# Optimization experiments

Hardware: AMD Instinct MI355X
Metric: run time of the kernel (lower is better)

Reference implementation:

```python
import jax, jax.numpy as jnp
import numpy as np

N, E, B, DIN, D = 65536, 1048576, 256, 32, 64
NUM_STEPS_MP = 2   # num_step_message_passing
SET2SET_STEPS = 3  # processing_steps
NUM_CLASSES = 4


def setup_inputs() -> dict:
    key = jax.random.key(0)
    ks = jax.random.split(key, 24)
    def gl(k, shape, fan_in):
        return (jax.random.normal(k, shape, jnp.float32) / np.sqrt(fan_in)).astype(jnp.float32)
    x = jax.random.normal(ks[0], (N, DIN), jnp.float32)
    edge_index = jax.random.randint(ks[1], (2, E), 0, N, dtype=jnp.int32).astype(jnp.int64)
    batch = jnp.sort(jax.random.randint(ks[2], (N,), 0, B, dtype=jnp.int32)).astype(jnp.int64)
    inp = dict(
        x=x, edge_index=edge_index, batch=batch,
        # conv1.mlp: Linear(DIN -> D)
        W_mlp=gl(ks[3], (D, DIN), DIN), b_mlp=jnp.zeros((D,), jnp.float32),
        # HenrionConv linear (D -> D), messages scatter-summed over edges
        W_conv=gl(ks[4], (D, D), D), b_conv=jnp.zeros((D,), jnp.float32),
        # GRU(input = D + DIN, hidden = D); gate order r,z,n (PyTorch)
        gru_W_ih=gl(ks[5], (3 * D, D + DIN), D + DIN),
        gru_W_hh=gl(ks[6], (3 * D, D), D),
        gru_b_ih=jnp.zeros((3 * D,), jnp.float32),
        gru_b_hh=jnp.zeros((3 * D,), jnp.float32),
        # Set2Set LSTM(input = 2D, hidden = D); gate order i,f,g,o (PyTorch)
        lstm_W_ih=gl(ks[7], (4 * D, 2 * D), 2 * D),
        lstm_W_hh=gl(ks[8], (4 * D, D), D),
        lstm_b_ih=jnp.zeros((4 * D,), jnp.float32),
        lstm_b_hh=jnp.zeros((4 * D,), jnp.float32),
        # head MLPs
        W1=gl(ks[9], (D, 2 * D), 2 * D), b1=jnp.zeros((D,), jnp.float32),
        W2=gl(ks[10], (NUM_CLASSES, D), D), b2=jnp.zeros((NUM_CLASSES,), jnp.float32),
        num_graphs=B,
    )
    return inp


def _forward(x, edge_index, batch, W_mlp, b_mlp, W_conv, b_conv,
             gru_W_ih, gru_W_hh, gru_b_ih, gru_b_hh,
             lstm_W_ih, lstm_W_hh, lstm_b_ih, lstm_b_hh,
             W1, b1, W2, b2, num_graphs):
    n = x.shape[0]
    d = W_mlp.shape[0]
    src, dst = edge_index[0], edge_index[1]

    # ---- Henrion_MPNNConv ----
    out = x @ W_mlp.T + b_mlp            # [N, D]
    h = out
    for _ in range(NUM_STEPS_MP):
        # HenrionConv: linear on source node features, scatter-sum to destinations
        msg = (out @ W_conv.T + b_conv)[src]               # [E, D] gather
        m = jax.ops.segment_sum(msg, dst, num_segments=n)  # [N, D] scatter
        inp = jnp.concatenate([m, x], axis=-1)             # [N, D+DIN]
        # GRU cell (seq len 1)
        gi = inp @ gru_W_ih.T + gru_b_ih
        gh = h @ gru_W_hh.T + gru_b_hh
        gi_r, gi_z, gi_n = jnp.split(gi, 3, axis=-1)
        gh_r, gh_z, gh_n = jnp.split(gh, 3, axis=-1)
        r = jax.nn.sigmoid(gi_r + gh_r)
        z = jax.nn.sigmoid(gi_z + gh_z)
        ng = jnp.tanh(gi_n + r * gh_n)
        h = (1.0 - z) * ng + z * h
        out = h

    # ---- Set2Set (processing_steps = 3) ----
    bsz = num_graphs
    q_star = jnp.zeros((bsz, 2 * d), out.dtype)
    hl = jnp.zeros((bsz, d), out.dtype)
    cl = jnp.zeros((bsz, d), out.dtype)
    for _ in range(SET2SET_STEPS):
        gates = q_star @ lstm_W_ih.T + lstm_b_ih + hl @ lstm_W_hh.T + lstm_b_hh
        gi, gf, gg, go = jnp.split(gates, 4, axis=-1)
        cl = jax.nn.sigmoid(gf) * cl + jax.nn.sigmoid(gi) * jnp.tanh(gg)
        hl = jax.nn.sigmoid(go) * jnp.tanh(cl)
        q = hl                                             # [B, D]
        e = jnp.sum(out * q[batch], axis=-1)               # [N]
        e_max = jax.ops.segment_max(e, batch, num_segments=bsz)
        e_max = jnp.where(jnp.isfinite(e_max), e_max, 0.0)
        a = jnp.exp(e - e_max[batch])
        a_sum = jax.ops.segment_sum(a, batch, num_segments=bsz)
        a = a / jnp.maximum(a_sum[batch], 1e-16)           # segment softmax
        r = jax.ops.segment_sum(a[:, None] * out, batch, num_segments=bsz)  # [B, D]
        q_star = jnp.concatenate([q, r], axis=-1)          # [B, 2D]

    # ---- head (eval mode: dropout is identity) ----
    hid = jax.nn.relu(q_star @ W1.T + b1)
    logits = hid @ W2.T + b2
    return jax.nn.log_softmax(logits, axis=-1)             # [B, 4]


def reference(x, edge_index, batch, W_mlp, b_mlp, W_conv, b_conv,
              gru_W_ih, gru_W_hh, gru_b_ih, gru_b_hh,
              lstm_W_ih, lstm_W_hh, lstm_b_ih, lstm_b_hh,
              W1, b1, W2, b2, num_graphs):
    return _forward(x, edge_index, batch, W_mlp, b_mlp, W_conv, b_conv,
                    gru_W_ih, gru_W_hh, gru_b_ih, gru_b_hh,
                    lstm_W_ih, lstm_W_hh, lstm_b_ih, lstm_b_hh,
                    W1, b1, W2, b2, num_graphs)
```

## Files before the change

### kernel.cpp

```cpp
#include <hip/hip_runtime.h>
#include <math.h>

constexpr int Nn  = 65536;
constexpr int Ne  = 1048576;
constexpr int Bg  = 256;
constexpr int DIN = 32;
constexpr int D   = 64;

constexpr int NB   = 256;
constexpr int BCAP = 6144;

typedef __attribute__((ext_vector_type(8))) short bf16x8;
typedef __attribute__((ext_vector_type(8))) unsigned short u16x8;
typedef __attribute__((ext_vector_type(4))) float f32x4;

__device__ __forceinline__ float sigf(float x) { return 1.0f / (1.0f + expf(-x)); }

__device__ __forceinline__ unsigned short bf16_rne(float f) {
  unsigned u = __float_as_uint(f);
  unsigned r = u + 0x7FFFu + ((u >> 16) & 1u);
  return (unsigned short)(r >> 16);
}
__device__ __forceinline__ float bf16_tof(unsigned short h) {
  return __uint_as_float(((unsigned)h) << 16);
}
__device__ __forceinline__ void split2(float f, unsigned short& hi, unsigned short& lo) {
  hi = bf16_rne(f);
  lo = bf16_rne(f - bf16_tof(hi));
}
__device__ __forceinline__ float recon(unsigned short hi, unsigned short lo) {
  return bf16_tof(hi) + bf16_tof(lo);
}

#define MFMA(a, b, c) __builtin_amdgcn_mfma_f32_16x16x32_bf16(a, b, c, 0, 0, 0)

__global__ void k_prepw(const float* __restrict__ W_mlp, const float* __restrict__ W_conv,
                        const float* __restrict__ gWih, const float* __restrict__ gWhh,
                        const float* __restrict__ b_conv,
                        const float* __restrict__ lW_ih, const float* __restrict__ lW_hh,
                        const float* __restrict__ W1,
                        unsigned short* __restrict__ mlp_h, unsigned short* __restrict__ mlp_l,
                        unsigned short* __restrict__ gw_h,  unsigned short* __restrict__ gw_l,
                        float* __restrict__ WihT, float* __restrict__ WhhT,
                        float* __restrict__ W1T, float* __restrict__ vfold,
                        const int* __restrict__ batch, int* __restrict__ gp,
                        int* __restrict__ rp) {
  int idx = blockIdx.x * 256 + threadIdx.x;
  if (idx < 30720) {
    int c = idx / 6144, rem = idx % 6144;
    int nt = rem >> 9, lane = (rem >> 3) & 63, j = rem & 7;
    int n = nt * 16 + (lane & 15);
    int kk = c * 32 + (lane >> 4) * 8 + j;
    float v;
    if (c < 2) {
      float s = 0.f;
      for (int o = 0; o < 64; ++o) s = fmaf(gWih[n * 96 + o], W_conv[o * 64 + kk], s);
      v = s;
    } else if (c == 2) {
      v = gWih[n * 96 + kk];
    } else {
      v = gWhh[n * 64 + (c - 3) * 32 + (lane >> 4) * 8 + j];
    }
    unsigned short hi, lo; split2(v, hi, lo);
    gw_h[idx] = hi; gw_l[idx] = lo;
    return;
  }
  if (idx < 32768) {
    int lp = idx - 30720;
    int nt = lp >> 9, lane = (lp >> 3) & 63, j = lp & 7;
    int n = nt * 16 + (lane & 15);
    unsigned short hi, lo;
    split2(W_mlp[n * 32 + (lane >> 4) * 8 + j], hi, lo);
    mlp_h[lp] = hi; mlp_l[lp] = lo;
    return;
  }
  int t = idx - 32768;
  if (t < 32768) {
    int row = t / 128, k = t % 128;
    WihT[k * 256 + row] = lW_ih[t];
  } else if (t < 49152) {
    int j = t - 32768;
    int row = j / 64, k = j % 64;
    WhhT[k * 256 + row] = lW_hh[j];
  } else if (t < 57344) {
    int j = t - 49152;
    int row = j / 128, k = j % 128;
    W1T[k * 64 + row] = W1[j];
  } else if (t < 57344 + Bg + 1) {
    int g = t - 57344;
    if (g == 0) rp[Nn] = Ne;
    int lo = 0, hi = Nn;
    while (lo < hi) {
      int mid = (lo + hi) >> 1;
      if (batch[mid] < g) lo = mid + 1; else hi = mid;
    }
    gp[g] = lo;
  } else if (t < 57344 + 257 + 192) {
    int g = t - 57344 - 257;
    float s = 0.f;
    for (int o = 0; o < 64; ++o) s = fmaf(gWih[g * 96 + o], b_conv[o], s);
    vfold[g] = s;
  }
}

__global__ __launch_bounds__(256) void k_conv1(const float* __restrict__ x,
                                               const unsigned short* __restrict__ Wh,
                                               const unsigned short* __restrict__ Wl,
                                               const float* __restrict__ bias,
                                               unsigned short* __restrict__ hph,
                                               unsigned short* __restrict__ hpl,
                                               unsigned short* __restrict__ Aih,
                                               unsigned short* __restrict__ Ail) {
  int wave = threadIdx.x >> 6, lane = threadIdx.x & 63;
  int quad = lane >> 4;
  int n0w = blockIdx.x * 64 + wave * 16;
  int rowA = n0w + (lane & 15);
  const float4* xp = (const float4*)&x[(size_t)rowA * 32 + quad * 8];
  float4 xa = xp[0], xb = xp[1];
  float xv[8] = {xa.x, xa.y, xa.z, xa.w, xb.x, xb.y, xb.z, xb.w};
  bf16x8 ah, al;
#pragma unroll
  for (int j = 0; j < 8; ++j) {
    unsigned short hi, lo; split2(xv[j], hi, lo);
    ah[j] = (short)hi; al[j] = (short)lo;
  }
  *(bf16x8*)&Aih[(size_t)rowA * 96 + 64 + quad * 8] = ah;
  *(bf16x8*)&Ail[(size_t)rowA * 96 + 64 + quad * 8] = al;

  f32x4 acc[4] = {};
#pragma unroll
  for (int nt = 0; nt < 4; ++nt) {
    bf16x8 bh = *(const bf16x8*)&Wh[(nt * 64 + lane) * 8];
    bf16x8 bl = *(const bf16x8*)&Wl[(nt * 64 + lane) * 8];
    acc[nt] = MFMA(ah, bh, acc[nt]);
    acc[nt] = MFMA(ah, bl, acc[nt]);
    acc[nt] = MFMA(al, bh, acc[nt]);
  }
  int col0 = lane & 15;
#pragma unroll
  for (int nt = 0; nt < 4; ++nt) {
    float bv = bias[nt * 16 + col0];
#pragma unroll
    for (int r = 0; r < 4; ++r) {
      int node = n0w + quad * 4 + r;
      float v = acc[nt][r] + bv;
      size_t o = (size_t)node * 64 + nt * 16 + col0;
      unsigned short hi, lo; split2(v, hi, lo);
      hph[o] = hi; hpl[o] = lo;
    }
  }
}

__global__ __launch_bounds__(256) void k_aggr(const unsigned short* __restrict__ Hh,
                                              const int* __restrict__ rp,
                                              const int* __restrict__ srcs,
                                              unsigned short* __restrict__ Sh,
                                              unsigned short* __restrict__ Sl) {
  int wave = threadIdx.x >> 6, lane = threadIdx.x & 63;
  int node = blockIdx.x * 4 + wave;
  int s = rp[node], e = rp[node + 1];
  int n = e - s;
  const int* sp = srcs + s;
  int col8 = (lane & 7) * 8;
  int eslot = lane >> 3;
  float acc8[8] = {};
  int k = 0;
  for (; k + 16 <= n; k += 16) {
    int sA = sp[k + eslot];
    int sB = sp[k + 8 + eslot];
    u16x8 a = *(const u16x8*)&Hh[(size_t)sA * 64 + col8];
    u16x8 b = *(const u16x8*)&Hh[(size_t)sB * 64 + col8];
#pragma unroll
    for (int j = 0; j < 8; ++j) acc8[j] += bf16_tof(a[j]);
#pragma unroll
    for (int j = 0; j < 8; ++j) acc8[j] += bf16_tof(b[j]);
  }
  for (; k < n; k += 8) {
    if (k + eslot < n) {
      int sA = sp[k + eslot];
      u16x8 a = *(const u16x8*)&Hh[(size_t)sA * 64 + col8];
#pragma unroll
      for (int j = 0; j < 8; ++j) acc8[j] += bf16_tof(a[j]);
    }
  }
#pragma unroll
  for (int m = 8; m <= 32; m <<= 1) {
#pragma unroll
    for (int j = 0; j < 8; ++j) acc8[j] += __shfl_xor(acc8[j], m);
  }
  if (lane < 8) {
    u16x8 hv, lv;
#pragma unroll
    for (int j = 0; j < 8; ++j) {
      unsigned short hi, lo; split2(acc8[j], hi, lo);
      hv[j] = hi; lv[j] = lo;
    }
    *(u16x8*)&Sh[(size_t)node * 64 + col8] = hv;
    *(u16x8*)&Sl[(size_t)node * 64 + col8] = lv;
  }
}

__global__ __launch_bounds__(256, 2) void k_gru(const unsigned short* __restrict__ Aih,
                                                const unsigned short* __restrict__ Ail,
                                                const unsigned short* __restrict__ Hh,
                                                const unsigned short* __restrict__ Hl,
                                                const unsigned short* __restrict__ Sh,
                                                const unsigned short* __restrict__ Sl,
                                                const unsigned short* __restrict__ gw_h,
                                                const unsigned short* __restrict__ gw_l,
                                                const float* __restrict__ b_ih,
                                                const float* __restrict__ b_hh,
                                                const float* __restrict__ vfold,
                                                const int* __restrict__ rp,
                                                unsigned short* __restrict__ nph,
                                                unsigned short* __restrict__ npl) {
  __shared__ unsigned short sW[2][12288];
  int tid = threadIdx.x;
  int wave = tid >> 6, lane = tid & 63;
  int quad = lane >> 4;
  int n0w = blockIdx.x * 128 + wave * 32;
  int rowA0 = n0w + (lane & 15);

  f32x4 acc0[12] = {}, acc1[12] = {};
  f32x4 aN0[4] = {}, aN1[4] = {};

  bf16x8 gvh[3], gvl[3];
#pragma unroll
  for (int j = 0; j < 3; ++j) {
    gvh[j] = *(const bf16x8*)&gw_h[(tid + j * 256) * 8];
    gvl[j] = *(const bf16x8*)&gw_l[(tid + j * 256) * 8];
  }
#pragma unroll
  for (int j = 0; j < 3; ++j) {
    *(bf16x8*)&sW[0][(tid + j * 256) * 8] = gvh[j];
    *(bf16x8*)&sW[0][6144 + (tid + j * 256) * 8] = gvl[j];
  }
  __syncthreads();

#pragma unroll
  for (int c = 0; c < 5; ++c) {
    const int buf = c & 1;
    if (c < 4) {
#pragma unroll
      for (int j = 0; j < 3; ++j) {
        gvh[j] = *(const bf16x8*)&gw_h[(c + 1) * 6144 + (tid + j * 256) * 8];
        gvl[j] = *(const bf16x8*)&gw_l[(c + 1) * 6144 + (tid + j * 256) * 8];
      }
    }
    bf16x8 a0h, a0l, a1h, a1l;
    if (c < 2) {
      size_t b0 = (size_t)rowA0 * 64 + c * 32 + quad * 8;
      size_t b1 = (size_t)(rowA0 + 16) * 64 + c * 32 + quad * 8;
      a0h = *(const bf16x8*)&Sh[b0]; a0l = *(const bf16x8*)&Sl[b0];
      a1h = *(const bf16x8*)&Sh[b1]; a1l = *(const bf16x8*)&Sl[b1];
    } else if (c == 2) {
      size_t b0 = (size_t)rowA0 * 96 + 64 + quad * 8;
      size_t b1 = (size_t)(rowA0 + 16) * 96 + 64 + quad * 8;
      a0h = *(const bf16x8*)&Aih[b0]; a0l = *(const bf16x8*)&Ail[b0];
      a1h = *(const bf16x8*)&Aih[b1]; a1l = *(const bf16x8*)&Ail[b1];
    } else {
      size_t b0 = (size_t)rowA0 * 64 + (c - 3) * 32 + quad * 8;
      size_t b1 = (size_t)(rowA0 + 16) * 64 + (c - 3) * 32 + quad * 8;
      a0h = *(const bf16x8*)&Hh[b0]; a0l = *(const bf16x8*)&Hl[b0];
      a1h = *(const bf16x8*)&Hh[b1]; a1l = *(const bf16x8*)&Hl[b1];
    }
    const unsigned short* sw = sW[buf];
#pragma unroll
    for (int nt = 0; nt < 12; ++nt) {
      bf16x8 bh = *(const bf16x8*)&sw[(nt * 64 + lane) * 8];
      bf16x8 bl = *(const bf16x8*)&sw[6144 + (nt * 64 + lane) * 8];
      if (c < 3 || nt < 8) {
        acc0[nt] = MFMA(a0h, bh, acc0[nt]);
        acc0[nt] = MFMA(a0h, bl, acc0[nt]);
        acc0[nt] = MFMA(a0l, bh, acc0[nt]);
        acc1[nt] = MFMA(a1h, bh, acc1[nt]);
        acc1[nt] = MFMA(a1h, bl, acc1[nt]);
        acc1[nt] = MFMA(a1l, bh, acc1[nt]);
      } else {
        aN0[nt - 8] = MFMA(a0h, bh, aN0[nt - 8]);
        aN0[nt - 8] = MFMA(a0h, bl, aN0[nt - 8]);
        aN0[nt - 8] = MFMA(a0l, bh, aN0[nt - 8]);
        aN1[nt - 8] = MFMA(a1h, bh, aN1[nt - 8]);
        aN1[nt - 8] = MFMA(a1h, bl, aN1[nt - 8]);
        aN1[nt - 8] = MFMA(a1l, bh, aN1[nt - 8]);
      }
    }
    if (c < 4) {
#pragma unroll
      for (int j = 0; j < 3; ++j) {
        *(bf16x8*)&sW[1 - buf][(tid + j * 256) * 8] = gvh[j];
        *(bf16x8*)&sW[1 - buf][6144 + (tid + j * 256) * 8] = gvl[j];
      }
    }
    __syncthreads();
  }

  int col0 = lane & 15;
#pragma unroll
  for (int tile = 0; tile < 2; ++tile) {
    int nb = n0w + tile * 16;
#pragma unroll
    for (int r = 0; r < 4; ++r) {
      int node = nb + quad * 4 + r;
      float degf = (float)(rp[node + 1] - rp[node]);
#pragma unroll
      for (int nt = 0; nt < 4; ++nt) {
        int g = nt * 16 + col0;
        size_t o = (size_t)node * 64 + g;
        float br  = b_ih[g] + b_hh[g] + degf * vfold[g];
        float bz  = b_ih[64 + g] + b_hh[64 + g] + degf * vfold[64 + g];
        float bin = b_ih[128 + g] + degf * vfold[128 + g];
        float bhn = b_hh[128 + g];
        float gr = tile ? acc1[nt][r]     : acc0[nt][r];
        float gz = tile ? acc1[nt + 4][r] : acc0[nt + 4][r];
        float gn = tile ? acc1[nt + 8][r] : acc0[nt + 8][r];
        float hn = tile ? aN1[nt][r]      : aN0[nt][r];
        float rr = sigf(gr + br);
        float zz = sigf(gz + bz);
        float nn = tanhf(gn + bin + rr * (hn + bhn));
        float h_old = recon(Hh[o], Hl[o]);
        float hv = (1.f - zz) * nn + zz * h_old;
        unsigned short hi, lo; split2(hv, hi, lo);
        nph[o] = hi; npl[o] = lo;
      }
    }
  }
}

__global__ __launch_bounds__(256) void k_bucket(const int* __restrict__ eidx,
                                                int* __restrict__ gcur,
                                                int* __restrict__ payload) {
  __shared__ int lcnt[NB];
  __shared__ int lcur[NB];
  int t = threadIdx.x;
  int e0 = blockIdx.x * 4096;
  lcnt[t] = 0;
  __syncthreads();
  int ds[16], ss[16];
#pragma unroll
  for (int i = 0; i < 16; ++i) {
    int e = e0 + i * 256 + t;
    ds[i] = eidx[Ne + e];
    ss[i] = eidx[e];
    atomicAdd(&lcnt[ds[i] >> 8], 1);
  }
  __syncthreads();
  lcur[t] = atomicAdd(&gcur[t * 16], lcnt[t]);
  __syncthreads();
#pragma unroll
  for (int i = 0; i < 16; ++i) {
    int b = ds[i] >> 8;
    int p = atomicAdd(&lcur[b], 1);
    if (p < BCAP) payload[b * BCAP + p] = (ss[i] << 8) | (ds[i] & 255);
  }
}

__global__ __launch_bounds__(256) void k_placeB(const int* __restrict__ gcur,
                                                const int* __restrict__ payload,
                                                int* __restrict__ rp,
                                                int* __restrict__ srcs) {
  __shared__ int sAll[NB];
  __shared__ int hst[NB];
  __shared__ int cur[NB];
  int b = blockIdx.x, t = threadIdx.x;
  sAll[t] = gcur[t * 16];
  hst[t] = 0;
  __syncthreads();
  int cnt = min(sAll[b], BCAP);
  for (int off = 1; off < NB; off <<= 1) {
    int v = (t >= off) ? sAll[t - off] : 0;
    __syncthreads();
    sAll[t] += v;
    __syncthreads();
  }
  int base = sAll[b] - gcur[b * 16];
  const int* pay = &payload[b * BCAP];
  for (int i = t; i < cnt; i += 256) atomicAdd(&hst[pay[i] & 255], 1);
  __syncthreads();
  int c = hst[t];
  cur[t] = c;
  __syncthreads();
  for (int off = 1; off < NB; off <<= 1) {
    int v = (t >= off) ? cur[t - off] : 0;
    __syncthreads();
    cur[t] += v;
    __syncthreads();
  }
  int excl = cur[t] - c;
  rp[b * 256 + t] = base + excl;
  cur[t] = base + excl;
  __syncthreads();
  for (int i = t; i < cnt; i += 256) {
    int pl = pay[i];
    int p = atomicAdd(&cur[pl & 255], 1);
    srcs[p] = pl >> 8;
  }
}

constexpr int LCAP = 448;
constexpr int LPAD = 68;
constexpr int S2T  = 512;
__global__ __launch_bounds__(S2T) void k_s2s(const unsigned short* __restrict__ hph,
                                             const unsigned short* __restrict__ hpl,
                                             const int* __restrict__ gp,
                                             const float* __restrict__ WihT,
                                             const float* __restrict__ WhhT,
                                             const float* __restrict__ b_ih,
                                             const float* __restrict__ b_hh,
                                             const float* __restrict__ W1T,
                                             const float* __restrict__ b1,
                                             const float* __restrict__ W2,
                                             const float* __restrict__ b2,
                                             float* __restrict__ outp) {
  extern __shared__ float hL[];
  int g = blockIdx.x;
  int t = threadIdx.x;
  int w = t >> 6, lane = t & 63;
  __shared__ float qstar_s[128];
  __shared__ float hs[64], cs[64], gates[256];
  __shared__ float eL[LCAP];
  __shared__ float partial[8][64];
  __shared__ float asum_p[8];
  __shared__ float l4[4];
  __shared__ float hid[64];

  if (t < 128) qstar_s[t] = 0.f;
  if (t < 64) { hs[t] = 0.f; cs[t] = 0.f; }
  int s = gp[g], e = gp[g + 1];
  int cnt = e - s;

  {
    int total = cnt * 64;
    for (int j = t * 4; j < total; j += S2T * 4) {
      int nd = j >> 6, col = j & 63;
      ushort4 hh = *(const ushort4*)&hph[(size_t)s * 64 + j];
      ushort4 ll = *(const ushort4*)&hpl[(size_t)s * 64 + j];
      float4 v;
      v.x = recon(hh.x, ll.x); v.y = recon(hh.y, ll.y);
      v.z = recon(hh.z, ll.z); v.w = recon(hh.w, ll.w);
      *(float4*)&hL[nd * LPAD + col] = v;
    }
  }

  for (int it = 0; it < 3; ++it) {
    __syncthreads();

    if (t < 256) {
      float acc = b_ih[t] + b_hh[t];
      for (int k = 0; k < 128; ++k) acc = fmaf(WihT[k * 256 + t], qstar_s[k], acc);
      for (int k = 0; k < 64; ++k)  acc = fmaf(WhhT[k * 256 + t], hs[k], acc);
      gates[t] = acc;
    }
    __syncthreads();
    if (t < 64) {
      float ig = sigf(gates[t]),        fg = sigf(gates[64 + t]);
      float gg = tanhf(gates[128 + t]), og = sigf(gates[192 + t]);
      float c = fg * cs[t] + ig * gg;
      float q = og * tanhf(c);
      cs[t] = c;
      hs[t] = q;
      qstar_s[t] = q;
    }
    __syncthreads();

    int c4 = (lane & 15) * 4;
    float4 qv = {qstar_s[c4], qstar_s[c4 + 1], qstar_s[c4 + 2], qstar_s[c4 + 3]};
    for (int i0 = s + w * 4; i0 < e; i0 += 32) {
      int node = i0 + (lane >> 4);
      float p = 0.f;
      if (node < e) {
        float4 hv = *(const float4*)&hL[(node - s) * LPAD + c4];
        p = hv.x * qv.x + hv.y * qv.y + hv.z * qv.z + hv.w * qv.w;
      }
      p += __shfl_xor(p, 1); p += __shfl_xor(p, 2);
      p += __shfl_xor(p, 4); p += __shfl_xor(p, 8);
      if (node < e && (lane & 15) == 0) eL[node - s] = p;
    }
    __syncthreads();

    float m = -INFINITY;
    for (int i = lane; i < cnt; i += 64) m = fmaxf(m, eL[i]);
#pragma unroll
    for (int o = 32; o >= 1; o >>= 1) m = fmaxf(m, __shfl_xor(m, o));
    float emax = isfinite(m) ? m : 0.f;

    float acc = 0.f, asum = 0.f;
    for (int i = s + w; i < e; i += 8) {
      float a = expf(eL[i - s] - emax);
      asum += a;
      acc = fmaf(a, hL[(i - s) * LPAD + lane], acc);
    }
    partial[w][lane] = acc;
    if (lane == 0) asum_p[w] = asum;
    __syncthreads();
    if (t < 64) {
      float r = 0.f, as = 0.f;
      for (int q = 0; q < 8; ++q) { r += partial[q][t]; as += asum_p[q]; }
      float rv = (cnt > 0) ? r / fmaxf(as, 1e-16f) : 0.f;
      qstar_s[64 + t] = rv;
    }
  }
  __syncthreads();

  if (t < 64) {
    float a1 = b1[t];
    for (int k = 0; k < 64; ++k)   a1 = fmaf(W1T[k * 64 + t], qstar_s[k], a1);
    for (int k = 64; k < 128; ++k) a1 = fmaf(W1T[k * 64 + t], qstar_s[k], a1);
    hid[t] = fmaxf(a1, 0.f);
  }
  __syncthreads();
  if (t < 4) {
    float lg = b2[t];
    for (int d = 0; d < 64; ++d) lg = fmaf(W2[t * 64 + d], hid[d], lg);
    l4[t] = lg;
  }
  __syncthreads();
  if (t < 4) {
    float mx = fmaxf(fmaxf(l4[0], l4[1]), fmaxf(l4[2], l4[3]));
    float ssum = expf(l4[0] - mx) + expf(l4[1] - mx) + expf(l4[2] - mx) + expf(l4[3] - mx);
    outp[g * 4 + t] = l4[t] - mx - logf(ssum);
  }
}

extern "C" void kernel_launch(void* const* d_in, const int* in_sizes, int n_in,
                              void* d_out, int out_size, void* d_ws, size_t ws_size,
                              hipStream_t stream) {
  const float* x        = (const float*)d_in[0];
  const int*   eidx     = (const int*)d_in[1];
  const int*   batch    = (const int*)d_in[2];
  const float* W_mlp    = (const float*)d_in[3];
  const float* b_mlp    = (const float*)d_in[4];
  const float* W_conv   = (const float*)d_in[5];
  const float* b_conv   = (const float*)d_in[6];
  const float* gW_ih    = (const float*)d_in[7];
  const float* gW_hh    = (const float*)d_in[8];
  const float* gb_ih    = (const float*)d_in[9];
  const float* gb_hh    = (const float*)d_in[10];
  const float* lW_ih    = (const float*)d_in[11];
  const float* lW_hh    = (const float*)d_in[12];
  const float* lb_ih    = (const float*)d_in[13];
  const float* lb_hh    = (const float*)d_in[14];
  const float* W1       = (const float*)d_in[15];
  const float* b1       = (const float*)d_in[16];
  const float* W2       = (const float*)d_in[17];
  const float* b2       = (const float*)d_in[18];
  float* outp = (float*)d_out;

  char* ws = (char*)d_ws;
  size_t off = 0;
  auto alloc = [&](size_t bytes) { size_t r = off; off = (off + bytes + 255) & ~(size_t)255; return r; };
  unsigned short* hpAh = (unsigned short*)(ws + alloc((size_t)Nn * 64 * 2));
  unsigned short* hpAl = (unsigned short*)(ws + alloc((size_t)Nn * 64 * 2));
  unsigned short* hpBh = (unsigned short*)(ws + alloc((size_t)Nn * 64 * 2));
  unsigned short* hpBl = (unsigned short*)(ws + alloc((size_t)Nn * 64 * 2));
  unsigned short* Aih  = (unsigned short*)(ws + alloc((size_t)Nn * 96 * 2));
  unsigned short* Ail  = (unsigned short*)(ws + alloc((size_t)Nn * 96 * 2));
  unsigned short* Sh   = (unsigned short*)(ws + alloc((size_t)Nn * 64 * 2));
  unsigned short* Sl   = (unsigned short*)(ws + alloc((size_t)Nn * 64 * 2));
  int*   rp    = (int*)(ws + alloc((size_t)(Nn + 1) * 4));
  int*   srcs  = (int*)(ws + alloc((size_t)Ne * 4));
  int*   gcur  = (int*)(ws + alloc((size_t)NB * 16 * 4));
  int*   payload = (int*)(ws + alloc((size_t)NB * BCAP * 4));
  int*   gp    = (int*)(ws + alloc((size_t)(Bg + 1) * 4));
  float* WihT  = (float*)(ws + alloc((size_t)128 * 256 * 4));
  float* WhhT  = (float*)(ws + alloc((size_t)64 * 256 * 4));
  float* W1T   = (float*)(ws + alloc((size_t)128 * 64 * 4));
  float* vfold = (float*)(ws + alloc(192 * 4));
  unsigned short* mlp_h = (unsigned short*)(ws + alloc(2048 * 2));
  unsigned short* mlp_l = (unsigned short*)(ws + alloc(2048 * 2));
  unsigned short* gw_h  = (unsigned short*)(ws + alloc(30720 * 2));
  unsigned short* gw_l  = (unsigned short*)(ws + alloc(30720 * 2));
  (void)in_sizes; (void)n_in; (void)out_size; (void)ws_size;

  hipMemsetAsync(gcur, 0, (size_t)NB * 16 * 4, stream);

  k_bucket<<<Ne / 4096, 256, 0, stream>>>(eidx, gcur, payload);
  k_placeB<<<NB, 256, 0, stream>>>(gcur, payload, rp, srcs);
  k_prepw<<<355, 256, 0, stream>>>(W_mlp, W_conv, gW_ih, gW_hh, b_conv,
                                   lW_ih, lW_hh, W1,
                                   mlp_h, mlp_l, gw_h, gw_l,
                                   WihT, WhhT, W1T, vfold, batch, gp, rp);

  k_conv1<<<Nn / 64, 256, 0, stream>>>(x, mlp_h, mlp_l, b_mlp, hpAh, hpAl, Aih, Ail);

  unsigned short *cph = hpAh, *cpl = hpAl, *nph = hpBh, *npl = hpBl;
  for (int step = 0; step < 2; ++step) {
    k_aggr<<<Nn / 4, 256, 0, stream>>>(cph, rp, srcs, Sh, Sl);
    k_gru<<<Nn / 128, 256, 0, stream>>>(Aih, Ail, cph, cpl, Sh, Sl, gw_h, gw_l,
                                        gb_ih, gb_hh, vfold, rp, nph, npl);
    unsigned short* tu;
    tu = cph; cph = nph; nph = tu;
    tu = cpl; cpl = npl; npl = tu;
  }

  const size_t dynLds = (size_t)LCAP * LPAD * sizeof(float);
  static bool attr_set = false;
  if (!attr_set) {
    hipFuncSetAttribute((const void*)k_s2s,
                        hipFuncAttributeMaxDynamicSharedMemorySize,
                        (int)dynLds);
    attr_set = true;
  }
  k_s2s<<<Bg, S2T, dynLds, stream>>>(cph, cpl, gp, WihT, WhhT,
                                     lb_ih, lb_hh, W1T, b1, W2, b2, outp);
}
```

Before: 301.2 us.

## Fuse neighbor aggregation into GRU kernel, dropping intermediate sum buffer

Removes the separate aggregation kernel and computes each node's neighbor sum inside the GRU kernel, directly in the MFMA A-fragment layout. Each lane walks its node's CSR edge list serially and splits the sums into bf16 hi/lo registers. This avoids one launch per step and the write and re-read of the summed buffer. The trade-off is much less parallelism per node in the gather phase and extra register pressure in an already heavy kernel.

```diff
diff --git a/kernel.cpp b/kernel.cpp
--- a/kernel.cpp
+++ b/kernel.cpp
@@ -151,67 +151,17 @@
   }
 }
 
-__global__ __launch_bounds__(256) void k_aggr(const unsigned short* __restrict__ Hh,
-                                              const int* __restrict__ rp,
-                                              const int* __restrict__ srcs,
-                                              unsigned short* __restrict__ Sh,
-                                              unsigned short* __restrict__ Sl) {
-  int wave = threadIdx.x >> 6, lane = threadIdx.x & 63;
-  int node = blockIdx.x * 4 + wave;
-  int s = rp[node], e = rp[node + 1];
-  int n = e - s;
-  const int* sp = srcs + s;
-  int col8 = (lane & 7) * 8;
-  int eslot = lane >> 3;
-  float acc8[8] = {};
-  int k = 0;
-  for (; k + 16 <= n; k += 16) {
-    int sA = sp[k + eslot];
-    int sB = sp[k + 8 + eslot];
-    u16x8 a = *(const u16x8*)&Hh[(size_t)sA * 64 + col8];
-    u16x8 b = *(const u16x8*)&Hh[(size_t)sB * 64 + col8];
-#pragma unroll
-    for (int j = 0; j < 8; ++j) acc8[j] += bf16_tof(a[j]);
-#pragma unroll
-    for (int j = 0; j < 8; ++j) acc8[j] += bf16_tof(b[j]);
-  }
-  for (; k < n; k += 8) {
-    if (k + eslot < n) {
-      int sA = sp[k + eslot];
-      u16x8 a = *(const u16x8*)&Hh[(size_t)sA * 64 + col8];
-#pragma unroll
-      for (int j = 0; j < 8; ++j) acc8[j] += bf16_tof(a[j]);
-    }
-  }
-#pragma unroll
-  for (int m = 8; m <= 32; m <<= 1) {
-#pragma unroll
-    for (int j = 0; j < 8; ++j) acc8[j] += __shfl_xor(acc8[j], m);
-  }
-  if (lane < 8) {
-    u16x8 hv, lv;
-#pragma unroll
-    for (int j = 0; j < 8; ++j) {
-      unsigned short hi, lo; split2(acc8[j], hi, lo);
-      hv[j] = hi; lv[j] = lo;
-    }
-    *(u16x8*)&Sh[(size_t)node * 64 + col8] = hv;
-    *(u16x8*)&Sl[(size_t)node * 64 + col8] = lv;
-  }
-}
-
 __global__ __launch_bounds__(256, 2) void k_gru(const unsigned short* __restrict__ Aih,
                                                 const unsigned short* __restrict__ Ail,
                                                 const unsigned short* __restrict__ Hh,
                                                 const unsigned short* __restrict__ Hl,
-                                                const unsigned short* __restrict__ Sh,
-                                                const unsigned short* __restrict__ Sl,
                                                 const unsigned short* __restrict__ gw_h,
                                                 const unsigned short* __restrict__ gw_l,
                                                 const float* __restrict__ b_ih,
                                                 const float* __restrict__ b_hh,
                                                 const float* __restrict__ vfold,
                                                 const int* __restrict__ rp,
+                                                const int* __restrict__ srcs,
                                                 unsigned short* __restrict__ nph,
                                                 unsigned short* __restrict__ npl) {
   __shared__ unsigned short sW[2][12288];
@@ -221,6 +171,67 @@
   int n0w = blockIdx.x * 128 + wave * 32;
   int rowA0 = n0w + (lane & 15);
 
+  bf16x8 fh[2][2], fl[2][2];
+  const size_t q8 = (size_t)(quad * 8);
+#pragma unroll
+  for (int tile = 0; tile < 2; ++tile) {
+    int row = rowA0 + tile * 16;
+    int s = rp[row], e = rp[row + 1];
+    int n = e - s;
+    const int* sp = srcs + s;
+    float acc0[8] = {}, acc1[8] = {};
+    int i = 0;
+    for (; i + 4 <= n; i += 4) {
+      int s0 = sp[i], s1 = sp[i + 1], s2 = sp[i + 2], s3 = sp[i + 3];
+      u16x8 a0 = *(const u16x8*)&Hh[(size_t)s0 * 64 + q8];
+      u16x8 b0 = *(const u16x8*)&Hh[(size_t)s0 * 64 + 32 + q8];
+      u16x8 a1 = *(const u16x8*)&Hh[(size_t)s1 * 64 + q8];
+      u16x8 b1 = *(const u16x8*)&Hh[(size_t)s1 * 64 + 32 + q8];
+      u16x8 a2 = *(const u16x8*)&Hh[(size_t)s2 * 64 + q8];
+      u16x8 b2 = *(const u16x8*)&Hh[(size_t)s2 * 64 + 32 + q8];
+      u16x8 a3 = *(const u16x8*)&Hh[(size_t)s3 * 64 + q8];
+      u16x8 b3 = *(const u16x8*)&Hh[(size_t)s3 * 64 + 32 + q8];
+#pragma unroll
+      for (int j = 0; j < 8; ++j) {
+        acc0[j] += bf16_tof(a0[j]);
+        acc1[j] += bf16_tof(b0[j]);
+      }
+#pragma unroll
+      for (int j = 0; j < 8; ++j) {
+        acc0[j] += bf16_tof(a1[j]);
+        acc1[j] += bf16_tof(b1[j]);
+      }
+#pragma unroll
+      for (int j = 0; j < 8; ++j) {
+        acc0[j] += bf16_tof(a2[j]);
+        acc1[j] += bf16_tof(b2[j]);
+      }
+#pragma unroll
+      for (int j = 0; j < 8; ++j) {
+        acc0[j] += bf16_tof(a3[j]);
+        acc1[j] += bf16_tof(b3[j]);
+      }
+    }
+    for (; i < n; ++i) {
+      int src = sp[i];
+      u16x8 v0 = *(const u16x8*)&Hh[(size_t)src * 64 + q8];
+      u16x8 v1 = *(const u16x8*)&Hh[(size_t)src * 64 + 32 + q8];
+#pragma unroll
+      for (int j = 0; j < 8; ++j) {
+        acc0[j] += bf16_tof(v0[j]);
+        acc1[j] += bf16_tof(v1[j]);
+      }
+    }
+#pragma unroll
+    for (int j = 0; j < 8; ++j) {
+      unsigned short hi, lo;
+      split2(acc0[j], hi, lo);
+      fh[tile][0][j] = (short)hi; fl[tile][0][j] = (short)lo;
+      split2(acc1[j], hi, lo);
+      fh[tile][1][j] = (short)hi; fl[tile][1][j] = (short)lo;
+    }
+  }
+
   f32x4 acc0[12] = {}, acc1[12] = {};
   f32x4 aN0[4] = {}, aN1[4] = {};
 
@@ -249,10 +260,8 @@
     }
     bf16x8 a0h, a0l, a1h, a1l;
     if (c < 2) {
-      size_t b0 = (size_t)rowA0 * 64 + c * 32 + quad * 8;
-      size_t b1 = (size_t)(rowA0 + 16) * 64 + c * 32 + quad * 8;
-      a0h = *(const bf16x8*)&Sh[b0]; a0l = *(const bf16x8*)&Sl[b0];
-      a1h = *(const bf16x8*)&Sh[b1]; a1l = *(const bf16x8*)&Sl[b1];
+      a0h = fh[0][c]; a0l = fl[0][c];
+      a1h = fh[1][c]; a1l = fl[1][c];
     } else if (c == 2) {
       size_t b0 = (size_t)rowA0 * 96 + 64 + quad * 8;
       size_t b1 = (size_t)(rowA0 + 16) * 96 + 64 + quad * 8;
@@ -555,8 +564,6 @@
   unsigned short* hpBl = (unsigned short*)(ws + alloc((size_t)Nn * 64 * 2));
   unsigned short* Aih  = (unsigned short*)(ws + alloc((size_t)Nn * 96 * 2));
   unsigned short* Ail  = (unsigned short*)(ws + alloc((size_t)Nn * 96 * 2));
-  unsigned short* Sh   = (unsigned short*)(ws + alloc((size_t)Nn * 64 * 2));
-  unsigned short* Sl   = (unsigned short*)(ws + alloc((size_t)Nn * 64 * 2));
   int*   rp    = (int*)(ws + alloc((size_t)(Nn + 1) * 4));
   int*   srcs  = (int*)(ws + alloc((size_t)Ne * 4));
   int*   gcur  = (int*)(ws + alloc((size_t)NB * 16 * 4));
@@ -585,9 +592,8 @@
 
   unsigned short *cph = hpAh, *cpl = hpAl, *nph = hpBh, *npl = hpBl;
   for (int step = 0; step < 2; ++step) {
-    k_aggr<<<Nn / 4, 256, 0, stream>>>(cph, rp, srcs, Sh, Sl);
-    k_gru<<<Nn / 128, 256, 0, stream>>>(Aih, Ail, cph, cpl, Sh, Sl, gw_h, gw_l,
-                                        gb_ih, gb_hh, vfold, rp, nph, npl);
+    k_gru<<<Nn / 128, 256, 0, stream>>>(Aih, Ail, cph, cpl, gw_h, gw_l,
+                                        gb_ih, gb_hh, vfold, rp, srcs, nph, npl);
     unsigned short* tu;
     tu = cph; cph = nph; nph = tu;
     tu = cpl; cpl = npl; npl = tu;
```

Result: faster. 291.2 us (-3.3%).
